# Performance work log

Hardware: AMD Instinct MI355X
Metric: run time of the kernel (lower is better)

## Reference

```python
import jax, jax.numpy as jnp
import numpy as np

EMBED_DIM = 1024
N_HEADS = 16
HEAD_DIM = EMBED_DIM // N_HEADS


def setup_inputs() -> dict:
    key = jax.random.key(0)
    ks = jax.random.split(key, 8)
    B, Tq, Tk, C = 2, 2048, 2048, EMBED_DIM
    s = 1.0 / np.sqrt(C)
    return {
        "query": jax.random.normal(ks[0], (B, Tq, C), jnp.float32),
        "context": jax.random.normal(ks[1], (B, Tk, C), jnp.float32),
        "Wq": jax.random.normal(ks[2], (C, C), jnp.float32) * s,
        "bq": jnp.zeros((C,), jnp.float32),
        "Wkv": jax.random.normal(ks[3], (C, 2 * C), jnp.float32) * s,
        "bkv": jnp.zeros((2 * C,), jnp.float32),
        "Wo": jax.random.normal(ks[4], (C, C), jnp.float32) * s,
        "bo": jnp.zeros((C,), jnp.float32),
    }


def reference(query, context, Wq, bq, Wkv, bkv, Wo, bo):
    B, Tq, C = query.shape
    Tk = context.shape[1]
    H, D = N_HEADS, HEAD_DIM
    # projections
    q = (query @ Wq + bq).reshape(B, Tq, H, D)        # [B,Tq,H,D]
    kv = (context @ Wkv + bkv).reshape(B, Tk, 2, H, D)
    k = kv[:, :, 0]                                   # [B,Tk,H,D]
    v = kv[:, :, 1]
    scale = D ** -0.5
    # attention scores [B,H,Tq,Tk]
    attn = jnp.einsum("bqhd,bkhd->bhqk", q, k) * scale
    attn = jax.nn.softmax(attn, axis=-1)
    # dropout p=0.0 -> identity in eval / p=0
    out = jnp.einsum("bhqk,bkhd->bqhd", attn, v).reshape(B, Tq, C)
    return out @ Wo + bo
```

## Files before the change

kernel.cpp:

```cpp
#include <hip/hip_runtime.h>
#include <math.h>

typedef unsigned short u16;
typedef unsigned int u32;
typedef __attribute__((ext_vector_type(8))) short short8;
typedef __attribute__((ext_vector_type(4))) short short4v;
typedef __attribute__((ext_vector_type(4))) float f32x4;

__device__ __forceinline__ u16 f2bf(float f) {
  union { float f; unsigned u; } x; x.f = f;
  unsigned r = x.u + 0x7FFFu + ((x.u >> 16) & 1u);
  return (u16)(r >> 16);
}

__device__ __forceinline__ u32 asu(float f) {
  union { float f; u32 u; } x; x.f = f; return x.u;
}

__device__ __forceinline__ u32 pack2bf(float a, float b) {
  return __builtin_amdgcn_perm(asu(b) + 0x8000u, asu(a) + 0x8000u, 0x07060302u);
}

__device__ __forceinline__ u32 cvtpk2bf(float a, float b) {
  u32 r;
  asm("v_cvt_pk_bf16_f32 %0, %1, %2" : "=v"(r) : "v"(a), "v"(b));
  return r;
}

__device__ __forceinline__ void gld_lds16(const void* g, void* l) {
  __builtin_amdgcn_global_load_lds(
      (const __attribute__((address_space(1))) unsigned int*)g,
      (__attribute__((address_space(3))) unsigned int*)l, 16, 0, 0);
}

__global__ void pre_kernel(const float* __restrict__ q, const float* __restrict__ c,
                           const float* __restrict__ Wq, const float* __restrict__ Wkv,
                           const float* __restrict__ Wo,
                           u16* __restrict__ xq, u16* __restrict__ xc,
                           u16* __restrict__ WqF, u16* __restrict__ WkvF,
                           u16* __restrict__ WoF) {
  __shared__ float tile[32][33];
  int bx = blockIdx.x;
  int t = threadIdx.y * 32 + threadIdx.x;
  if (bx < 8192) {
    int i = bx * 256 + t;
    const float* src = q; u16* dst = xq;
    if (i >= 1048576) { i -= 1048576; src = c; dst = xc; }
    float4 v = ((const float4*)src)[i];
    ((uint2*)dst)[i] = make_uint2(
        (unsigned)f2bf(v.x) | ((unsigned)f2bf(v.y) << 16),
        (unsigned)f2bf(v.z) | ((unsigned)f2bf(v.w) << 16));
  } else {
    int g = bx - 8192;
    int gx = g & 127, gy = g >> 7;
    const float* src; u16* dst; int N, n0;
    if (gx < 32)      { src = Wq;  dst = WqF;  N = 1024; n0 = gx * 32; }
    else if (gx < 96) { src = Wkv; dst = WkvF; N = 2048; n0 = (gx - 32) * 32; }
    else              { src = Wo;  dst = WoF;  N = 1024; n0 = (gx - 96) * 32; }
    int k0 = gy * 32;
    int tx = threadIdx.x, ty = threadIdx.y;
#pragma unroll
    for (int i = 0; i < 4; ++i)
      tile[ty * 4 + i][tx] = src[(size_t)(k0 + ty * 4 + i) * N + n0 + tx];
    __syncthreads();
    int e = t * 4;
    int ch = e >> 9, rem = e & 511;
    int kg = (rem >> 7) & 3;
    int nl = (rem >> 3) & 15;
    int j0 = rem & 7;
    int kk = kg * 8 + j0;
    int nn = ch * 16 + nl;
    u32 lo = pack2bf(tile[kk][nn], tile[kk + 1][nn]);
    u32 hi = pack2bf(tile[kk + 2][nn], tile[kk + 3][nn]);
    *(uint2*)(dst + (size_t)(((n0 >> 4) + ch) * 32 + gy) * 512 + rem) = make_uint2(lo, hi);
  }
}

__global__ __launch_bounds__(256) void qkv_gemm(
    const u16* __restrict__ Xq, const u16* __restrict__ Xc,
    const u16* __restrict__ WqF, const u16* __restrict__ WkvF,
    const float* __restrict__ bq, const float* __restrict__ bkv,
    u16* __restrict__ qb, u16* __restrict__ kf, u16* __restrict__ vf,
    float qscale) {
  __shared__ __align__(16) u16 smem[16896];
  const int tid = threadIdx.x, lane = tid & 63, wave = tid >> 6;
  const int quad = lane >> 4, cl = lane & 15;
  const int wr = (wave >> 1) * 64, wc = (wave & 1) * 64;

  const int xcd = blockIdx.x & 7, pos = blockIdx.x >> 3;
  const u16 *A, *Bf; const float* bias; int m0, n0; bool isq;
  if (pos < 64) {
    isq = false; A = Xc; Bf = WkvF; bias = bkv;
    m0 = ((xcd >> 1) * 8 + (pos >> 3)) * 128;
    n0 = ((xcd & 1) * 8 + (pos & 7)) * 128;
  } else {
    int p = pos - 64;
    isq = true;  A = Xq; Bf = WqF;  bias = bq;
    m0 = (xcd * 4 + (p >> 3)) * 128;
    n0 = (p & 7) * 128;
  }
  const int bn4 = (n0 + wc) >> 4;

  const int rA = lane >> 3;
  const int kcs = ((lane & 7) ^ rA) * 8;
  const int r7 = cl & 7;

  auto stageA = [&](int k0, int buf) {
    u16* As = smem + buf * 8192;
#pragma unroll
    for (int it = 0; it < 4; ++it) {
      int chunk = it * 4 + wave;
      gld_lds16(A + (size_t)(m0 + chunk * 8 + rA) * 1024 + k0 + kcs, As + chunk * 512);
    }
  };

  f32x4 acc[4][4] = {};

  stageA(0, 0);
  __syncthreads();

  for (int i = 0; i < 16; ++i) {
    const int k0 = i * 64;
    const int cur = i & 1;
    if (i < 15) stageA(k0 + 64, cur ^ 1);
    const u16* As = smem + cur * 8192;
    short8 bf[2][4];
#pragma unroll
    for (int ks = 0; ks < 2; ++ks)
#pragma unroll
      for (int ni = 0; ni < 4; ++ni)
        bf[ks][ni] = *(const short8*)(Bf + (size_t)((bn4 + ni) * 32 + (k0 >> 5) + ks) * 512 + lane * 8);
#pragma unroll
    for (int ks = 0; ks < 2; ++ks) {
      short8 af[4];
#pragma unroll
      for (int mi = 0; mi < 4; ++mi) {
        int row = wr + mi * 16 + cl;
        af[mi] = *(const short8*)(As + (row >> 3) * 512 + r7 * 64 +
                                  (((ks << 2) | quad) ^ r7) * 8);
      }
#pragma unroll
      for (int mi = 0; mi < 4; ++mi)
#pragma unroll
        for (int ni = 0; ni < 4; ++ni)
          acc[mi][ni] = __builtin_amdgcn_mfma_f32_16x16x32_bf16(af[mi], bf[ks][ni], acc[mi][ni], 0, 0, 0);
    }
    __syncthreads();
  }

  if (isq) {
#pragma unroll
    for (int mi = 0; mi < 4; ++mi)
#pragma unroll
      for (int ni = 0; ni < 4; ++ni)
#pragma unroll
        for (int r = 0; r < 4; ++r) {
          int row = m0 + wr + mi * 16 + quad * 4 + r;
          int col = n0 + wc + ni * 16 + cl;
          qb[(size_t)row * 1024 + col] = f2bf((acc[mi][ni][r] + bias[col]) * qscale);
        }
    return;
  }

  const int b = m0 >> 11, kt0 = (m0 & 2047) >> 6;
  const bool kreg = (n0 < 1024);
  if (kreg) {
#pragma unroll
    for (int mi = 0; mi < 4; ++mi)
#pragma unroll
      for (int ni = 0; ni < 4; ++ni)
#pragma unroll
        for (int r = 0; r < 4; ++r)
          smem[(wr + mi * 16 + quad * 4 + r) * 132 + wc + ni * 16 + cl] =
              f2bf(acc[mi][ni][r] + bias[n0 + wc + ni * 16 + cl]);
    __syncthreads();
#pragma unroll
    for (int i = 0; i < 8; ++i) {
      int c = i * 4 + wave;
      int hs = c >> 4, ts = (c >> 3) & 1, ks = (c >> 2) & 1, idx = c & 3;
      int h = (n0 >> 6) + hs;
      size_t bhkt = ((size_t)((b * 16 + h) * 32 + kt0 + ts)) * 4096;
      short8 v = *(const short8*)(smem + (ts * 64 + idx * 16 + cl) * 132 +
                                  hs * 64 + ks * 32 + quad * 8);
      *(short8*)(kf + bhkt + (size_t)(ks * 4 + idx) * 512 + lane * 8) = v;
    }
  } else {
#pragma unroll
    for (int mi = 0; mi < 4; ++mi)
#pragma unroll
      for (int ni = 0; ni < 4; ++ni) {
        float v0 = acc[mi][ni][0] + bias[n0 + wc + ni * 16 + cl];
        float v1 = acc[mi][ni][1] + bias[n0 + wc + ni * 16 + cl];
        float v2 = acc[mi][ni][2] + bias[n0 + wc + ni * 16 + cl];
        float v3 = acc[mi][ni][3] + bias[n0 + wc + ni * 16 + cl];
        *(uint2*)(smem + (wc + ni * 16 + cl) * 132 + wr + mi * 16 + quad * 4) =
            make_uint2(pack2bf(v0, v1), pack2bf(v2, v3));
      }
    __syncthreads();
#pragma unroll
    for (int i = 0; i < 8; ++i) {
      int c = i * 4 + wave;
      int hs = c >> 4, ts = (c >> 3) & 1, ks = (c >> 2) & 1, idx = c & 3;
      int h = ((n0 - 1024) >> 6) + hs;
      size_t bhkt = ((size_t)((b * 16 + h) * 32 + kt0 + ts)) * 4096;
      const u16* src = smem + (hs * 64 + idx * 16 + cl) * 132 + ts * 64 + ks * 32 + quad * 4;
      short8 v;
      *(short4v*)&v       = *(const short4v*)(src);
      *((short4v*)&v + 1) = *(const short4v*)(src + 16);
      *(short8*)(vf + bhkt + (size_t)(ks * 4 + idx) * 512 + lane * 8) = v;
    }
  }
}

__global__ __launch_bounds__(256) void o_gemm(
    const u16* __restrict__ A, const u16* __restrict__ Bf,
    const float* __restrict__ bias, float* __restrict__ Cm) {
  __shared__ __align__(16) u16 smem[24576];
  const int tid = threadIdx.x, lane = tid & 63, wave = tid >> 6;
  const int quad = lane >> 4, cl = lane & 15;
  const int xcd = blockIdx.x & 7, pos = blockIdx.x >> 3;
  const int m0 = (xcd * 8 + (pos >> 3)) * 64, n0 = (pos & 7) * 128;
  const int wr = (wave >> 1) * 32, wc = (wave & 1) * 64;
  const int n04 = n0 >> 4;

  const int rA = lane >> 3;
  const int kcs = ((lane & 7) ^ rA) * 8;
  const int r7 = cl & 7;

  auto stageA = [&](int k0, int buf) {
    u16* As = smem + buf * 4096;
#pragma unroll
    for (int it = 0; it < 2; ++it) {
      int chunk = wave * 2 + it;
      gld_lds16(A + (size_t)(m0 + chunk * 8 + rA) * 1024 + k0 + kcs, As + chunk * 512);
    }
  };
  auto stageB = [&](int k0, int buf) {
    u16* Bs = smem + 8192 + buf * 8192;
    const int k05 = k0 >> 5;
#pragma unroll
    for (int it = 0; it < 4; ++it) {
      int c = it * 4 + wave;
      int j = c >> 1, ks = c & 1;
      gld_lds16(Bf + (size_t)((n04 + j) * 32 + k05 + ks) * 512 + lane * 8, Bs + c * 512);
    }
  };

  f32x4 acc[2][4] = {};

  stageA(0, 0);
  stageB(0, 0);
  __syncthreads();

  for (int i = 0; i < 16; ++i) {
    const int k0 = i * 64;
    const int cur = i & 1;
    if (i < 15) { stageA(k0 + 64, cur ^ 1); stageB(k0 + 64, cur ^ 1); }
    const u16* As = smem + cur * 4096;
    const u16* Bs = smem + 8192 + cur * 8192;
    short8 bf[2][4];
#pragma unroll
    for (int ks = 0; ks < 2; ++ks)
#pragma unroll
      for (int ni = 0; ni < 4; ++ni)
        bf[ks][ni] = *(const short8*)(Bs + (size_t)((((wave & 1) * 4 + ni) * 2 + ks) * 512) + lane * 8);
#pragma unroll
    for (int ks = 0; ks < 2; ++ks) {
      short8 af[2];
#pragma unroll
      for (int mi = 0; mi < 2; ++mi) {
        int row = wr + mi * 16 + cl;
        af[mi] = *(const short8*)(As + (row >> 3) * 512 + r7 * 64 +
                                  (((ks << 2) | quad) ^ r7) * 8);
      }
#pragma unroll
      for (int mi = 0; mi < 2; ++mi)
#pragma unroll
        for (int ni = 0; ni < 4; ++ni)
          acc[mi][ni] = __builtin_amdgcn_mfma_f32_16x16x32_bf16(af[mi], bf[ks][ni], acc[mi][ni], 0, 0, 0);
    }
    __syncthreads();
  }
#pragma unroll
  for (int mi = 0; mi < 2; ++mi)
#pragma unroll
    for (int ni = 0; ni < 4; ++ni)
#pragma unroll
      for (int r = 0; r < 4; ++r) {
        int row = m0 + wr + mi * 16 + quad * 4 + r;
        int col = n0 + wc + ni * 16 + cl;
        Cm[(size_t)row * 1024 + col] = acc[mi][ni][r] + bias[col];
      }
}

__global__ __launch_bounds__(512, 4) void flash_attn(
    const u16* __restrict__ qb, const u16* __restrict__ kf,
    const u16* __restrict__ vf, u16* __restrict__ outp) {
  __shared__ __align__(16) u16 kv[2][16 * 512];
  const int tid = threadIdx.x, lane = tid & 63, wave = tid >> 6;
  const int quad = lane >> 4, cl = lane & 15;
  const int id = blockIdx.x;
  const int h = (id & 7) | (((id >> 3) & 1) << 3);
  const int b = (id >> 4) & 1;
  const int qt = id >> 5;

  const int qrow0 = b * 2048 + qt * 128 + wave * 16;
  short8 bq[2];
#pragma unroll
  for (int ks = 0; ks < 2; ++ks)
    bq[ks] = *(const short8*)(qb + (size_t)(qrow0 + cl) * 1024 + h * 64 + ks * 32 + quad * 8);

  short8 ones;
#pragma unroll
  for (int j = 0; j < 8; ++j) ones[j] = (short)0x3F80;

  const u16* kfb = kf + (size_t)((b * 16 + h) * 32) * 4096;
  const u16* vfb = vf + (size_t)((b * 16 + h) * 32) * 4096;

  auto stage = [&](int kt, int buf) {
#pragma unroll
    for (int i = 0; i < 2; ++i) {
      int c = wave * 2 + i;
      const u16* src = (c < 8) ? (kfb + (size_t)kt * 4096 + c * 512)
                               : (vfb + (size_t)kt * 4096 + (c - 8) * 512);
      gld_lds16(src + lane * 8, &kv[buf][c * 512]);
    }
  };

  f32x4 o_acc[4] = {};
  f32x4 l_acc = {};

  stage(0, 0);
  __syncthreads();

#pragma unroll 1
  for (int kt = 0; kt < 32; ++kt) {
    const int cur = kt & 1, nxt = cur ^ 1;
    if (kt < 31) stage(kt + 1, nxt);
    const u16* kb = &kv[cur][0];
    const u16* vb = &kv[cur][8 * 512];
    f32x4 st[4] = {};
    __builtin_amdgcn_s_setprio(1);
#pragma unroll
    for (int ks = 0; ks < 2; ++ks)
#pragma unroll
      for (int ni = 0; ni < 4; ++ni) {
        short8 ak = *(const short8*)(kb + (ks * 4 + ni) * 512 + lane * 8);
        st[ni] = __builtin_amdgcn_mfma_f32_16x16x32_bf16(ak, bq[ks], st[ni], 0, 0, 0);
      }
    __builtin_amdgcn_s_setprio(0);
    short8 av[2][4];
#pragma unroll
    for (int ks = 0; ks < 2; ++ks)
#pragma unroll
      for (int nd = 0; nd < 4; ++nd)
        av[ks][nd] = *(const short8*)(vb + (ks * 4 + nd) * 512 + lane * 8);
    u32 bp[2][4];
#pragma unroll
    for (int ni = 0; ni < 4; ++ni) {
      float p0 = __builtin_amdgcn_exp2f(st[ni][0]);
      float p1 = __builtin_amdgcn_exp2f(st[ni][1]);
      float p2 = __builtin_amdgcn_exp2f(st[ni][2]);
      float p3 = __builtin_amdgcn_exp2f(st[ni][3]);
      bp[ni >> 1][(ni & 1) * 2 + 0] = cvtpk2bf(p0, p1);
      bp[ni >> 1][(ni & 1) * 2 + 1] = cvtpk2bf(p2, p3);
    }
    __builtin_amdgcn_s_setprio(1);
#pragma unroll
    for (int ks = 0; ks < 2; ++ks) {
      short8 pb;
      *(u32*)&pb     = bp[ks][0];
      ((u32*)&pb)[1] = bp[ks][1];
      ((u32*)&pb)[2] = bp[ks][2];
      ((u32*)&pb)[3] = bp[ks][3];
#pragma unroll
      for (int nd = 0; nd < 4; ++nd)
        o_acc[nd] = __builtin_amdgcn_mfma_f32_16x16x32_bf16(av[ks][nd], pb, o_acc[nd], 0, 0, 0);
      l_acc = __builtin_amdgcn_mfma_f32_16x16x32_bf16(ones, pb, l_acc, 0, 0, 0);
    }
    __builtin_amdgcn_s_setprio(0);
    __syncthreads();
  }
  float inv = 1.f / l_acc[0];
  u16* Ow = &kv[0][wave * 16 * 68];
#pragma unroll
  for (int nd = 0; nd < 4; ++nd)
#pragma unroll
    for (int r2 = 0; r2 < 2; ++r2)
      *(u32*)(Ow + cl * 68 + nd * 16 + quad * 4 + r2 * 2) =
          cvtpk2bf(o_acc[nd][r2 * 2] * inv, o_acc[nd][r2 * 2 + 1] * inv);
#pragma unroll
  for (int half = 0; half < 2; ++half) {
    int row = half * 8 + (lane >> 3);
    int d0 = (lane & 7) * 8;
    short8 ov = *(const short8*)(Ow + row * 68 + d0);
    *(short8*)(outp + (size_t)(qrow0 + row) * 1024 + h * 64 + d0) = ov;
  }
}

extern "C" void kernel_launch(void* const* d_in, const int* in_sizes, int n_in,
                              void* d_out, int out_size, void* d_ws, size_t ws_size,
                              hipStream_t stream) {
  const float* query   = (const float*)d_in[0];
  const float* context = (const float*)d_in[1];
  const float* Wq  = (const float*)d_in[2];
  const float* bq  = (const float*)d_in[3];
  const float* Wkv = (const float*)d_in[4];
  const float* bkv = (const float*)d_in[5];
  const float* Wo  = (const float*)d_in[6];
  const float* bo  = (const float*)d_in[7];
  float* out = (float*)d_out;

  char* ws = (char*)d_ws;
  size_t off = 0;
  auto alloc = [&](size_t bytes) {
    char* p = ws + off;
    off += (bytes + 255) & ~(size_t)255;
    return p;
  };
  u16* buf0 = (u16*)alloc(4096ull * 1024 * 2);
  u16* xcb  = (u16*)alloc(4096ull * 1024 * 2);
  u16* WqF  = (u16*)alloc(1024ull * 1024 * 2);
  u16* WkvF = (u16*)alloc(2048ull * 1024 * 2);
  u16* WoF  = (u16*)alloc(1024ull * 1024 * 2);
  u16* qb   = (u16*)alloc(4096ull * 1024 * 2);
  u16* kfr  = (u16*)alloc(4ull * 1024 * 1024 * 2);
  u16* vfr  = (u16*)alloc(4ull * 1024 * 1024 * 2);

  const float QSCALE = 0.125f * 1.44269504f;

  pre_kernel<<<12288, dim3(32, 8), 0, stream>>>(query, context, Wq, Wkv, Wo,
                                                buf0, xcb, WqF, WkvF, WoF);
  qkv_gemm<<<768, 256, 0, stream>>>(buf0, xcb, WqF, WkvF, bq, bkv,
                                    qb, kfr, vfr, QSCALE);
  flash_attn<<<512, 512, 0, stream>>>(qb, kfr, vfr, buf0);
  o_gemm<<<512, 256, 0, stream>>>(buf0, WoF, bo, out);
}
```

Measured before the change: 190.9 us.

## Stage weight tiles through LDS and halve K-step in projection GEMM

The projection GEMM now loads the pre-packed weight fragments into shared memory with async global-to-LDS copies, double-buffered alongside the activation tile, instead of each wave reading B fragments directly from global memory. The K step per iteration drops from 64 to 32, giving twice as many iterations with half-size A buffers and a new swizzle. This is meant to share B loads across the waves of a block and cut redundant global traffic. In exchange it adds more barriers per K and a shorter MFMA chain between syncs.

```diff
diff --git a/kernel.cpp b/kernel.cpp
--- a/kernel.cpp
+++ b/kernel.cpp
@@ -99,52 +99,55 @@
     m0 = (xcd * 4 + (p >> 3)) * 128;
     n0 = (p & 7) * 128;
   }
-  const int bn4 = (n0 + wc) >> 4;
-
-  const int rA = lane >> 3;
-  const int kcs = ((lane & 7) ^ rA) * 8;
-  const int r7 = cl & 7;
+  const int n04 = n0 >> 4;
+
+  const int rA2 = lane >> 2;
+  const int kcs2 = ((lane & 3) ^ ((lane >> 3) & 3)) * 8;
 
   auto stageA = [&](int k0, int buf) {
-    u16* As = smem + buf * 8192;
-#pragma unroll
-    for (int it = 0; it < 4; ++it) {
-      int chunk = it * 4 + wave;
-      gld_lds16(A + (size_t)(m0 + chunk * 8 + rA) * 1024 + k0 + kcs, As + chunk * 512);
+    u16* As = smem + buf * 4096;
+#pragma unroll
+    for (int it = 0; it < 2; ++it) {
+      int c = wave * 2 + it;
+      gld_lds16(A + (size_t)(m0 + c * 16 + rA2) * 1024 + k0 + kcs2, As + c * 512);
+    }
+  };
+  auto stageB = [&](int k5, int buf) {
+    u16* Bs = smem + 8192 + buf * 4096;
+#pragma unroll
+    for (int it = 0; it < 2; ++it) {
+      int j = wave * 2 + it;
+      gld_lds16(Bf + (size_t)((n04 + j) * 32 + k5) * 512 + lane * 8, Bs + j * 512);
     }
   };
 
   f32x4 acc[4][4] = {};
 
   stageA(0, 0);
+  stageB(0, 0);
   __syncthreads();
 
-  for (int i = 0; i < 16; ++i) {
-    const int k0 = i * 64;
+  for (int i = 0; i < 32; ++i) {
     const int cur = i & 1;
-    if (i < 15) stageA(k0 + 64, cur ^ 1);
-    const u16* As = smem + cur * 8192;
-    short8 bf[2][4];
-#pragma unroll
-    for (int ks = 0; ks < 2; ++ks)
+    if (i < 31) { stageA((i + 1) * 32, cur ^ 1); stageB(i + 1, cur ^ 1); }
+    const u16* As = smem + cur * 4096;
+    const u16* Bs = smem + 8192 + cur * 4096;
+    short8 bf[4];
+#pragma unroll
+    for (int ni = 0; ni < 4; ++ni)
+      bf[ni] = *(const short8*)(Bs + (((wave & 1) * 4 + ni) * 512) + lane * 8);
+    short8 af[4];
+#pragma unroll
+    for (int mi = 0; mi < 4; ++mi) {
+      int row = wr + mi * 16 + cl;
+      af[mi] = *(const short8*)(As + (row >> 4) * 512 + cl * 32 +
+                                ((quad ^ ((cl >> 1) & 3)) * 8));
+    }
+#pragma unroll
+    for (int mi = 0; mi < 4; ++mi)
 #pragma unroll
       for (int ni = 0; ni < 4; ++ni)
-        bf[ks][ni] = *(const short8*)(Bf + (size_t)((bn4 + ni) * 32 + (k0 >> 5) + ks) * 512 + lane * 8);
-#pragma unroll
-    for (int ks = 0; ks < 2; ++ks) {
-      short8 af[4];
-#pragma unroll
-      for (int mi = 0; mi < 4; ++mi) {
-        int row = wr + mi * 16 + cl;
-        af[mi] = *(const short8*)(As + (row >> 3) * 512 + r7 * 64 +
-                                  (((ks << 2) | quad) ^ r7) * 8);
-      }
-#pragma unroll
-      for (int mi = 0; mi < 4; ++mi)
-#pragma unroll
-        for (int ni = 0; ni < 4; ++ni)
-          acc[mi][ni] = __builtin_amdgcn_mfma_f32_16x16x32_bf16(af[mi], bf[ks][ni], acc[mi][ni], 0, 0, 0);
-    }
+        acc[mi][ni] = __builtin_amdgcn_mfma_f32_16x16x32_bf16(af[mi], bf[ni], acc[mi][ni], 0, 0, 0);
     __syncthreads();
   }
 
```

New measurement: 192.7 us. About the same (+0.9%).
